# Kernel optimization log

Hardware: AMD Instinct MI355X
Metric: run time of the kernel (lower is better)

Reference implementation:

```python
import jax, jax.numpy as jnp
import numpy as np

T = 4096
STATE_DIM = 400
EMBED_DIM = 300
WIDTH_DIM = 20
HID = 150
GI_DIM = 2 * STATE_DIM + EMBED_DIM + WIDTH_DIM
BINS = (1, 2, 3, 4, 8, 16, 32, 64)
MAX_W = 10


def _dtoi(d):
    return sum(1 for b in BINS if d >= b)


def _mlp(x, W1, b1, W2, b2, W3, b3):
    h = jax.nn.relu(x @ W1 + b1)
    h = jax.nn.relu(h @ W2 + b2)
    return h @ W3 + b3


def setup_inputs() -> dict:
    key = jax.random.key(0)
    ks = jax.random.split(key, 16)
    s = 0.02
    return {
        "embeds": jax.random.normal(ks[0], (T, EMBED_DIM), jnp.float32),
        "states": jax.random.normal(ks[1], (T, STATE_DIM), jnp.float32),
        # attention Scorer (state_dim -> 150 -> 150 -> 1)
        "aW1": jax.random.normal(ks[2], (STATE_DIM, HID), jnp.float32) * s,
        "ab1": jnp.zeros((HID,), jnp.float32),
        "aW2": jax.random.normal(ks[3], (HID, HID), jnp.float32) * s,
        "ab2": jnp.zeros((HID,), jnp.float32),
        "aW3": jax.random.normal(ks[4], (HID, 1), jnp.float32) * s,
        "ab3": jnp.zeros((1,), jnp.float32),
        # width embedding table: len(BINS)+1 rows
        "width_table": jax.random.normal(ks[5], (len(BINS) + 1, WIDTH_DIM), jnp.float32) * s,
        # sm Scorer (gi_dim -> 150 -> 150 -> 1)
        "sW1": jax.random.normal(ks[6], (GI_DIM, HID), jnp.float32) * s,
        "sb1": jnp.zeros((HID,), jnp.float32),
        "sW2": jax.random.normal(ks[7], (HID, HID), jnp.float32) * s,
        "sb2": jnp.zeros((HID,), jnp.float32),
        "sW3": jax.random.normal(ks[8], (HID, 1), jnp.float32) * s,
        "sb3": jnp.zeros((1,), jnp.float32),
    }


def reference(embeds, states, aW1, ab1, aW2, ab2, aW3, ab3, width_table,
              sW1, sb1, sW2, sb2, sW3, sb3):
    t = states.shape[0]
    attn_scores = _mlp(states, aW1, ab1, aW2, ab2, aW3, ab3)[:, 0]  # [T]

    gs_parts, width_parts = [], []
    for n in range(1, MAX_W + 1):  # fixed, small window-size loop
        w = t - n + 1
        starts = jnp.arange(w)
        idx = starts[:, None] + jnp.arange(n)[None, :]        # [W, n]
        a = jax.nn.softmax(attn_scores[idx], axis=1)           # per-span softmax
        pooled = jnp.einsum('wn,wnd->wd', a, embeds[idx])      # [W, embed]
        g = jnp.concatenate([states[starts], states[starts + n - 1], pooled], axis=1)
        gs_parts.append(g)
        width_parts.append(width_table[_dtoi(n)][None, :].repeat(w, axis=0))

    gs = jnp.concatenate(gs_parts, axis=0)                     # [S, 2*state+embed]
    widths = jnp.concatenate(width_parts, axis=0)              # [S, width_dim]
    gs = jnp.concatenate([gs, widths], axis=1)                 # [S, gi_dim]
    sms = _mlp(gs, sW1, sb1, sW2, sb2, sW3, sb3)[:, 0]         # [S]
    return sms
```

## Files before the change

### kernel.cpp

```cpp
#include <hip/hip_runtime.h>
#include <hip/hip_bf16.h>

#define T_TOK 4096
#define HID   150
#define HPAD  160
#define NSPAN 40915
#define MAXW  10
#define NT    10

typedef __attribute__((ext_vector_type(8))) _Float16 f16x8;
typedef __attribute__((ext_vector_type(4))) float    f32x4;

__global__ __launch_bounds__(256) void k_prep(
    const float* __restrict__ aW1, const float* __restrict__ sW1,
    const float* __restrict__ aW2, const float* __restrict__ sW2,
    const float* __restrict__ wt, const float* __restrict__ sb1,
    _Float16* __restrict__ fW1, _Float16* __restrict__ fA1,
    _Float16* __restrict__ fB1, _Float16* __restrict__ fE1,
    _Float16* __restrict__ fA2, _Float16* __restrict__ fW2,
    float* __restrict__ wc)
{
    const int b = blockIdx.x;
    const int w = threadIdx.x >> 6, l = threadIdx.x & 63;

    if (b < 148) {
        int tw = b * 4 + w;
        if (tw >= 590) return;
        const float* src; int srcK, off; _Float16* d;
        if      (tw < 130) { src = aW1;             srcK = 400; off = 0;   d = fW1; }
        else if (tw < 260) { src = sW1;             srcK = 400; off = 130; d = fA1; }
        else if (tw < 390) { src = sW1 + 400 * HID; srcK = 400; off = 260; d = fB1; }
        else if (tw < 490) { src = sW1 + 800 * HID; srcK = 300; off = 390; d = fE1; }
        else if (tw < 540) { src = aW2;             srcK = 150; off = 490; d = fA2; }
        else               { src = sW2;             srcK = 150; off = 540; d = fW2; }
        int tb = tw - off;
        int kt = tb / NT, nt = tb - kt * NT;
        int n = nt * 16 + (l & 15);
        int kbase = kt * 32 + (l >> 4) * 8;
        f16x8 hv;
#pragma unroll
        for (int e = 0; e < 8; e++) {
            int k = kbase + e;
            float f = (k < srcK && n < HID) ? src[(size_t)k * HID + n] : 0.f;
            hv[e] = (_Float16)f;
        }
        *(f16x8*)(d + ((size_t)tb * 64 + l) * 8) = hv;
    } else {
        int n = b - 147;
        int c = threadIdx.x;
        if (c >= HPAD) return;
        float s = 0.f;
        if (c < HID) {
            const int dt[11] = {0, 1, 2, 3, 4, 4, 4, 4, 5, 5, 5};
            const float* ww = wt + dt[n] * 20;
            s = sb1[c];
#pragma unroll
            for (int j = 0; j < 20; j++) s = fmaf(ww[j], sW1[(1100 + j) * HID + c], s);
        }
        wc[(n - 1) * HPAD + c] = s;
    }
}

__global__ __launch_bounds__(256) void k_proj(
    const float* __restrict__ states, const float* __restrict__ embeds,
    const _Float16* __restrict__ fW1, const _Float16* __restrict__ fA1,
    const _Float16* __restrict__ fB1, const _Float16* __restrict__ fE1,
    const _Float16* __restrict__ fA2,
    const float* __restrict__ ab1, const float* __restrict__ ab2,
    const float* __restrict__ aW3, const float* __restrict__ ab3,
    _Float16* __restrict__ Abuf, _Float16* __restrict__ Bbuf,
    _Float16* __restrict__ Ebuf, float* __restrict__ scores)
{
    __shared__ alignas(16) _Float16 hh[5120];
    __shared__ float red[4][16];

    const float* Asrc; int lda, srcK, KT; const _Float16* Bf; _Float16* C = nullptr;
    switch (blockIdx.y) {
        case 0: Asrc = states; lda = 400; srcK = 400; KT = 13; Bf = fW1; break;
        case 1: Asrc = states; lda = 400; srcK = 400; KT = 13; Bf = fA1; C = Abuf; break;
        case 2: Asrc = states; lda = 400; srcK = 400; KT = 13; Bf = fB1; C = Bbuf; break;
        default:Asrc = embeds; lda = 300; srcK = 300; KT = 10; Bf = fE1; C = Ebuf; break;
    }
    const int w = threadIdx.x >> 6, l = threadIdx.x & 63;
    const int mtl = w >> 1;
    const int mt  = blockIdx.x * 2 + mtl;
    const int nh  = w & 1;
    const int m15 = l & 15;
    const int koff = (l >> 4) * 8;
    const float* arow = Asrc + (size_t)(mt * 16 + m15) * lda;
    const f16x8* pB = (const f16x8*)Bf;

    f32x4 acc[5];
#pragma unroll
    for (int c = 0; c < 5; c++) acc[c] = (f32x4){0.f, 0.f, 0.f, 0.f};

#pragma unroll 2
    for (int kt = 0; kt < KT; ++kt) {
        const int kbase = kt * 32 + koff;
        f16x8 a;
        if (kbase + 8 <= srcK) {
            float4 v0 = *(const float4*)(arow + kbase);
            float4 v1 = *(const float4*)(arow + kbase + 4);
            a[0] = (_Float16)v0.x; a[1] = (_Float16)v0.y;
            a[2] = (_Float16)v0.z; a[3] = (_Float16)v0.w;
            a[4] = (_Float16)v1.x; a[5] = (_Float16)v1.y;
            a[6] = (_Float16)v1.z; a[7] = (_Float16)v1.w;
        } else {
#pragma unroll
            for (int e = 0; e < 8; e++)
                a[e] = (_Float16)((kbase + e < srcK) ? arow[kbase + e] : 0.f);
        }
#pragma unroll
        for (int c = 0; c < 5; c++) {
            f16x8 bv = pB[(size_t)(kt * NT + nh * 5 + c) * 64 + l];
            acc[c] = __builtin_amdgcn_mfma_f32_16x16x32_f16(a, bv, acc[c], 0, 0, 0);
        }
    }

    if (blockIdx.y != 0) {
        const int m0 = mt * 16;
#pragma unroll
        for (int c = 0; c < 5; c++) {
            int col = (nh * 5 + c) * 16 + m15;
#pragma unroll
            for (int r = 0; r < 4; r++) {
                int row = m0 + (l >> 4) * 4 + r;
                C[(size_t)row * HPAD + col] = (_Float16)acc[c][r];
            }
        }
        return;
    }

#pragma unroll
    for (int c = 0; c < 5; c++) {
        int u   = nh * 5 + c;
        int col = u * 16 + m15;
        float bb = (col < HID) ? ab1[col] : 0.f;
        int kt = u >> 1;
        int g  = (u & 1) * 2 + (m15 >> 3);
        int e  = m15 & 7;
#pragma unroll
        for (int r = 0; r < 4; r++) {
            int rloc = (l >> 4) * 4 + r;
            float v = fmaxf(acc[c][r] + bb, 0.f);
            hh[((mtl * 5 + kt) * 64 + g * 16 + rloc) * 8 + e] = (_Float16)v;
        }
    }
    __syncthreads();

    const f16x8* pH = (const f16x8*)hh;
    const f16x8* pB2 = (const f16x8*)fA2;
    f32x4 acc2[5];
#pragma unroll
    for (int c = 0; c < 5; c++) acc2[c] = (f32x4){0.f, 0.f, 0.f, 0.f};
#pragma unroll
    for (int kt = 0; kt < 5; ++kt) {
        f16x8 a = pH[(mtl * 5 + kt) * 64 + l];
#pragma unroll
        for (int c = 0; c < 5; c++) {
            f16x8 bv = pB2[(size_t)(kt * NT + nh * 5 + c) * 64 + l];
            acc2[c] = __builtin_amdgcn_mfma_f32_16x16x32_f16(a, bv, acc2[c], 0, 0, 0);
        }
    }
    float p[4] = {0.f, 0.f, 0.f, 0.f};
#pragma unroll
    for (int c = 0; c < 5; c++) {
        int col = (nh * 5 + c) * 16 + m15;
        float bb = (col < HID) ? ab2[col] : 0.f;
        float wv = (col < HID) ? aW3[col] : 0.f;
#pragma unroll
        for (int r = 0; r < 4; r++) {
            float v = fmaxf(acc2[c][r] + bb, 0.f);
            p[r] = fmaf(v, wv, p[r]);
        }
    }
#pragma unroll
    for (int off = 1; off < 16; off <<= 1)
#pragma unroll
        for (int r = 0; r < 4; r++) p[r] += __shfl_xor(p[r], off);
    if (m15 == 0)
#pragma unroll
        for (int r = 0; r < 4; r++) red[w][(l >> 4) * 4 + r] = p[r];
    __syncthreads();
    if (threadIdx.x < 32) {
        int ml = threadIdx.x;
        scores[blockIdx.x * 32 + ml] =
            red[(ml >> 4) * 2 + 0][ml & 15] + red[(ml >> 4) * 2 + 1][ml & 15] + ab3[0];
    }
}

__global__ __launch_bounds__(256) void k_spanfinal(
    const float* __restrict__ scores, const _Float16* __restrict__ Abuf,
    const _Float16* __restrict__ Bbuf, const _Float16* __restrict__ Ebuf,
    const float* __restrict__ wc,
    const _Float16* __restrict__ fW2,
    const float* __restrict__ sb2, const float* __restrict__ sW3,
    const float* __restrict__ sb3, float* __restrict__ out)
{
    __shared__ alignas(16) _Float16 hh[5120];
    __shared__ float wg[32][10];
    __shared__ int   stI[32], nnI[32];
    __shared__ float red[4][16];

    const int tid = threadIdx.x;
    const int s0  = blockIdx.x * 32;

    if (tid < 32) {
        int span = s0 + tid;
        int n = 1, start = 0;
        if (span < NSPAN) {
            int base = 0;
#pragma unroll
            for (int i = 1; i <= MAXW; i++) {
                int ww = T_TOK - i + 1;
                if (span < base + ww) { n = i; break; }
                base += ww;
            }
            start = span - base;
        }
        float sc[MAXW]; float mx = -1e30f;
#pragma unroll
        for (int i = 0; i < MAXW; i++) {
            sc[i] = (i < n) ? scores[start + i] : -1e30f;
            mx = fmaxf(mx, sc[i]);
        }
        float ssum = 0.f;
#pragma unroll
        for (int i = 0; i < MAXW; i++) { sc[i] = __expf(sc[i] - mx); ssum += sc[i]; }
        float inv = 1.f / ssum;
#pragma unroll
        for (int i = 0; i < MAXW; i++) wg[tid][i] = (i < n) ? sc[i] * inv : 0.f;
        stI[tid] = start;
        nnI[tid] = n;
    }
    __syncthreads();

#pragma unroll
    for (int it = 0; it < 3; ++it) {
        int task = it * 256 + tid;
        if (task < 640) {
            int sl = task / 20;
            int q  = task - sl * 20;
            int start = stI[sl];
            int nn = nnI[sl];
            int d0 = q * 8;
            f16x8 a8 = *(const f16x8*)(Abuf + (size_t)start * HPAD + d0);
            f16x8 b8 = *(const f16x8*)(Bbuf + (size_t)(start + nn - 1) * HPAD + d0);
            const float* wr = wc + (nn - 1) * HPAD + d0;
            float v[8];
#pragma unroll
            for (int e = 0; e < 8; e++) v[e] = (float)a8[e] + (float)b8[e] + wr[e];
#pragma unroll
            for (int i = 0; i < MAXW; i++) {
                int ridx = min(start + i, T_TOK - 1);
                f16x8 e8 = *(const f16x8*)(Ebuf + (size_t)ridx * HPAD + d0);
                float aa = wg[sl][i];
#pragma unroll
                for (int e = 0; e < 8; e++) v[e] = fmaf(aa, (float)e8[e], v[e]);
            }
            f16x8 hv;
#pragma unroll
            for (int e = 0; e < 8; e++) hv[e] = (_Float16)fmaxf(v[e], 0.f);
            int mtl = sl >> 4, smr = sl & 15;
            int kt = q >> 2, gg = q & 3;
            *(f16x8*)(hh + ((mtl * 5 + kt) * 64 + gg * 16 + smr) * 8) = hv;
        }
    }
    __syncthreads();

    const int w = tid >> 6, l = tid & 63;
    const int mtl = w >> 1, nh = w & 1;
    const int m15 = l & 15;
    const f16x8* pH = (const f16x8*)hh;
    const f16x8* pB = (const f16x8*)fW2;
    f32x4 acc[5];
#pragma unroll
    for (int c = 0; c < 5; c++) acc[c] = (f32x4){0.f, 0.f, 0.f, 0.f};
#pragma unroll
    for (int kt = 0; kt < 5; ++kt) {
        f16x8 a = pH[(mtl * 5 + kt) * 64 + l];
#pragma unroll
        for (int c = 0; c < 5; c++) {
            f16x8 bv = pB[(size_t)(kt * NT + nh * 5 + c) * 64 + l];
            acc[c] = __builtin_amdgcn_mfma_f32_16x16x32_f16(a, bv, acc[c], 0, 0, 0);
        }
    }
    float p[4] = {0.f, 0.f, 0.f, 0.f};
#pragma unroll
    for (int c = 0; c < 5; c++) {
        int col = (nh * 5 + c) * 16 + m15;
        float bb = (col < HID) ? sb2[col] : 0.f;
        float wv = (col < HID) ? sW3[col] : 0.f;
#pragma unroll
        for (int r = 0; r < 4; r++) {
            float v = fmaxf(acc[c][r] + bb, 0.f);
            p[r] = fmaf(v, wv, p[r]);
        }
    }
#pragma unroll
    for (int off = 1; off < 16; off <<= 1)
#pragma unroll
        for (int r = 0; r < 4; r++) p[r] += __shfl_xor(p[r], off);
    if (m15 == 0)
#pragma unroll
        for (int r = 0; r < 4; r++) red[w][(l >> 4) * 4 + r] = p[r];
    __syncthreads();
    if (tid < 32) {
        int row = s0 + tid;
        if (row < NSPAN)
            out[row] = red[(tid >> 4) * 2 + 0][tid & 15] +
                       red[(tid >> 4) * 2 + 1][tid & 15] + sb3[0];
    }
}

extern "C" void kernel_launch(void* const* d_in, const int* in_sizes, int n_in,
                              void* d_out, int out_size, void* d_ws, size_t ws_size,
                              hipStream_t stream) {
    const float* embeds = (const float*)d_in[0];
    const float* states = (const float*)d_in[1];
    const float* aW1 = (const float*)d_in[2];
    const float* ab1 = (const float*)d_in[3];
    const float* aW2 = (const float*)d_in[4];
    const float* ab2 = (const float*)d_in[5];
    const float* aW3 = (const float*)d_in[6];
    const float* ab3 = (const float*)d_in[7];
    const float* wt  = (const float*)d_in[8];
    const float* sW1 = (const float*)d_in[9];
    const float* sb1 = (const float*)d_in[10];
    const float* sW2 = (const float*)d_in[11];
    const float* sb2 = (const float*)d_in[12];
    const float* sW3 = (const float*)d_in[13];
    const float* sb3 = (const float*)d_in[14];
    float* out = (float*)d_out;

    char* W = (char*)d_ws;
    _Float16* Abuf = (_Float16*)(W + 0);
    _Float16* Bbuf = (_Float16*)(W + 1310720);
    _Float16* Ebuf = (_Float16*)(W + 2621440);
    float* scores  = (float*)(W + 3932160);
    float* wcbuf   = (float*)(W + 3948544);
    _Float16* fW1  = (_Float16*)(W + 3954944);
    _Float16* fA1  = (_Float16*)(W + 4088064);
    _Float16* fB1  = (_Float16*)(W + 4221184);
    _Float16* fE1  = (_Float16*)(W + 4354304);
    _Float16* fA2  = (_Float16*)(W + 4456704);
    _Float16* fW2  = (_Float16*)(W + 4507904);

    k_prep<<<158, 256, 0, stream>>>(aW1, sW1, aW2, sW2, wt, sb1,
                                    fW1, fA1, fB1, fE1, fA2, fW2, wcbuf);
    k_proj<<<dim3(128, 4), 256, 0, stream>>>(states, embeds,
        fW1, fA1, fB1, fE1, fA2, ab1, ab2, aW3, ab3, Abuf, Bbuf, Ebuf, scores);
    k_spanfinal<<<1279, 256, 0, stream>>>(scores, Abuf, Bbuf, Ebuf, wcbuf,
        fW2, sb2, sW3, sb3, out);
}
```

Measured before the change: 38.42 us.

## Fuse projection and span-scoring kernels into one tile-local kernel with halo recompute

```diff
diff --git a/kernel.cpp b/kernel.cpp
--- a/kernel.cpp
+++ b/kernel.cpp
@@ -10,6 +10,23 @@
 
 typedef __attribute__((ext_vector_type(8))) _Float16 f16x8;
 typedef __attribute__((ext_vector_type(4))) float    f32x4;
+
+static __device__ __forceinline__ f16x8 cvt8(const float* __restrict__ row, int kbase, int K) {
+    f16x8 a;
+    if (kbase + 8 <= K) {
+        float4 v0 = *(const float4*)(row + kbase);
+        float4 v1 = *(const float4*)(row + kbase + 4);
+        a[0] = (_Float16)v0.x; a[1] = (_Float16)v0.y;
+        a[2] = (_Float16)v0.z; a[3] = (_Float16)v0.w;
+        a[4] = (_Float16)v1.x; a[5] = (_Float16)v1.y;
+        a[6] = (_Float16)v1.z; a[7] = (_Float16)v1.w;
+    } else {
+#pragma unroll
+        for (int e = 0; e < 8; e++)
+            a[e] = (_Float16)((kbase + e < K) ? row[kbase + e] : 0.f);
+    }
+    return a;
+}
 
 __global__ __launch_bounds__(256) void k_prep(
     const float* __restrict__ aW1, const float* __restrict__ sW1,
@@ -61,167 +78,160 @@
     }
 }
 
-__global__ __launch_bounds__(256) void k_proj(
+__global__ __launch_bounds__(256, 2) void k_main(
     const float* __restrict__ states, const float* __restrict__ embeds,
     const _Float16* __restrict__ fW1, const _Float16* __restrict__ fA1,
     const _Float16* __restrict__ fB1, const _Float16* __restrict__ fE1,
-    const _Float16* __restrict__ fA2,
+    const _Float16* __restrict__ fA2, const _Float16* __restrict__ fW2,
     const float* __restrict__ ab1, const float* __restrict__ ab2,
     const float* __restrict__ aW3, const float* __restrict__ ab3,
-    _Float16* __restrict__ Abuf, _Float16* __restrict__ Bbuf,
-    _Float16* __restrict__ Ebuf, float* __restrict__ scores)
+    const float* __restrict__ wcbuf, const float* __restrict__ sb2,
+    const float* __restrict__ sW3, const float* __restrict__ sb3,
+    float* __restrict__ out)
 {
-    __shared__ alignas(16) _Float16 hh[5120];
-    __shared__ float red[4][16];
-
-    const float* Asrc; int lda, srcK, KT; const _Float16* Bf; _Float16* C = nullptr;
-    switch (blockIdx.y) {
-        case 0: Asrc = states; lda = 400; srcK = 400; KT = 13; Bf = fW1; break;
-        case 1: Asrc = states; lda = 400; srcK = 400; KT = 13; Bf = fA1; C = Abuf; break;
-        case 2: Asrc = states; lda = 400; srcK = 400; KT = 13; Bf = fB1; C = Bbuf; break;
-        default:Asrc = embeds; lda = 300; srcK = 300; KT = 10; Bf = fE1; C = Ebuf; break;
-    }
-    const int w = threadIdx.x >> 6, l = threadIdx.x & 63;
-    const int mtl = w >> 1;
-    const int mt  = blockIdx.x * 2 + mtl;
-    const int nh  = w & 1;
-    const int m15 = l & 15;
+    __shared__ alignas(16) char smem[71808];
+    _Float16* Sf    = (_Float16*)(smem);
+    _Float16* Atile = (_Float16*)(smem + 26624);
+    _Float16* Btile = (_Float16*)(smem + 36864);
+    _Float16* Etile = (_Float16*)(smem + 47104);
+    _Float16* hh1   = (_Float16*)(smem + 57344);
+    float*    wg    = (float*)   (smem + 67584);
+    float*    scl   = (float*)   (smem + 70784);
+    float*    red   = (float*)   (smem + 70912);
+    float*    redB  = (float*)   (smem + 71552);
+
+    const int tid  = threadIdx.x;
+    const int w    = tid >> 6, l = tid & 63;
+    const int mtl  = w >> 1, nh = w & 1, m15 = l & 15;
     const int koff = (l >> 4) * 8;
-    const float* arow = Asrc + (size_t)(mt * 16 + m15) * lda;
-    const f16x8* pB = (const f16x8*)Bf;
-
-    f32x4 acc[5];
-#pragma unroll
-    for (int c = 0; c < 5; c++) acc[c] = (f32x4){0.f, 0.f, 0.f, 0.f};
-
+    const int t0   = blockIdx.x * 8;
+
+    for (int ft = w; ft < 26; ft += 4) {
+        int mt2 = ft / 13, kt = ft - mt2 * 13;
+        int row = min(t0 + mt2 * 16 + m15, T_TOK - 1);
+        f16x8 a = cvt8(states + (size_t)row * 400, kt * 32 + koff, 400);
+        *(f16x8*)(Sf + ((size_t)ft * 64 + l) * 8) = a;
+    }
+    __syncthreads();
+
+    for (int g = 0; g < 3; ++g) {
+        const f16x8* pB = (const f16x8*)(g == 0 ? fW1 : (g == 1 ? fA1 : fB1));
+        f32x4 acc[5];
+#pragma unroll
+        for (int c = 0; c < 5; c++) acc[c] = (f32x4){0.f, 0.f, 0.f, 0.f};
+#pragma unroll
+        for (int kt = 0; kt < 13; ++kt) {
+            f16x8 a = *(const f16x8*)(Sf + (((mtl * 13 + kt) * 64) + l) * 8);
+#pragma unroll
+            for (int c = 0; c < 5; c++) {
+                f16x8 bv = pB[(size_t)(kt * NT + nh * 5 + c) * 64 + l];
+                acc[c] = __builtin_amdgcn_mfma_f32_16x16x32_f16(a, bv, acc[c], 0, 0, 0);
+            }
+        }
+        if (g == 0) {
+#pragma unroll
+            for (int c = 0; c < 5; c++) {
+                int u = nh * 5 + c;
+                int col = u * 16 + m15;
+                float bb = (col < HID) ? ab1[col] : 0.f;
+                int kt2 = u >> 1;
+                int gg = (u & 1) * 2 + (m15 >> 3);
+                int e = m15 & 7;
+#pragma unroll
+                for (int r = 0; r < 4; r++) {
+                    int rloc = (l >> 4) * 4 + r;
+                    float v = fmaxf(acc[c][r] + bb, 0.f);
+                    hh1[((mtl * 5 + kt2) * 64 + gg * 16 + rloc) * 8 + e] = (_Float16)v;
+                }
+            }
+        } else {
+            _Float16* Tt = (g == 1) ? Atile : Btile;
+#pragma unroll
+            for (int c = 0; c < 5; c++) {
+                int col = (nh * 5 + c) * 16 + m15;
+#pragma unroll
+                for (int r = 0; r < 4; r++) {
+                    int rr = mtl * 16 + (l >> 4) * 4 + r;
+                    Tt[rr * HPAD + col] = (_Float16)acc[c][r];
+                }
+            }
+        }
+    }
+    {
+        f32x4 acc[5];
+#pragma unroll
+        for (int c = 0; c < 5; c++) acc[c] = (f32x4){0.f, 0.f, 0.f, 0.f};
+        int row = min(t0 + mtl * 16 + m15, T_TOK - 1);
+        const float* arow = embeds + (size_t)row * 300;
 #pragma unroll 2
-    for (int kt = 0; kt < KT; ++kt) {
-        const int kbase = kt * 32 + koff;
-        f16x8 a;
-        if (kbase + 8 <= srcK) {
-            float4 v0 = *(const float4*)(arow + kbase);
-            float4 v1 = *(const float4*)(arow + kbase + 4);
-            a[0] = (_Float16)v0.x; a[1] = (_Float16)v0.y;
-            a[2] = (_Float16)v0.z; a[3] = (_Float16)v0.w;
-            a[4] = (_Float16)v1.x; a[5] = (_Float16)v1.y;
-            a[6] = (_Float16)v1.z; a[7] = (_Float16)v1.w;
-        } else {
-#pragma unroll
-            for (int e = 0; e < 8; e++)
-                a[e] = (_Float16)((kbase + e < srcK) ? arow[kbase + e] : 0.f);
-        }
-#pragma unroll
-        for (int c = 0; c < 5; c++) {
-            f16x8 bv = pB[(size_t)(kt * NT + nh * 5 + c) * 64 + l];
-            acc[c] = __builtin_amdgcn_mfma_f32_16x16x32_f16(a, bv, acc[c], 0, 0, 0);
-        }
-    }
-
-    if (blockIdx.y != 0) {
-        const int m0 = mt * 16;
+        for (int kt = 0; kt < 10; ++kt) {
+            f16x8 a = cvt8(arow, kt * 32 + koff, 300);
+#pragma unroll
+            for (int c = 0; c < 5; c++) {
+                f16x8 bv = ((const f16x8*)fE1)[(size_t)(kt * NT + nh * 5 + c) * 64 + l];
+                acc[c] = __builtin_amdgcn_mfma_f32_16x16x32_f16(a, bv, acc[c], 0, 0, 0);
+            }
+        }
 #pragma unroll
         for (int c = 0; c < 5; c++) {
             int col = (nh * 5 + c) * 16 + m15;
 #pragma unroll
             for (int r = 0; r < 4; r++) {
-                int row = m0 + (l >> 4) * 4 + r;
-                C[(size_t)row * HPAD + col] = (_Float16)acc[c][r];
-            }
-        }
-        return;
-    }
-
-#pragma unroll
-    for (int c = 0; c < 5; c++) {
-        int u   = nh * 5 + c;
-        int col = u * 16 + m15;
-        float bb = (col < HID) ? ab1[col] : 0.f;
-        int kt = u >> 1;
-        int g  = (u & 1) * 2 + (m15 >> 3);
-        int e  = m15 & 7;
-#pragma unroll
-        for (int r = 0; r < 4; r++) {
-            int rloc = (l >> 4) * 4 + r;
-            float v = fmaxf(acc[c][r] + bb, 0.f);
-            hh[((mtl * 5 + kt) * 64 + g * 16 + rloc) * 8 + e] = (_Float16)v;
-        }
-    }
-    __syncthreads();
-
-    const f16x8* pH = (const f16x8*)hh;
-    const f16x8* pB2 = (const f16x8*)fA2;
-    f32x4 acc2[5];
-#pragma unroll
-    for (int c = 0; c < 5; c++) acc2[c] = (f32x4){0.f, 0.f, 0.f, 0.f};
-#pragma unroll
-    for (int kt = 0; kt < 5; ++kt) {
-        f16x8 a = pH[(mtl * 5 + kt) * 64 + l];
+                int rr = mtl * 16 + (l >> 4) * 4 + r;
+                Etile[rr * HPAD + col] = (_Float16)acc[c][r];
+            }
+        }
+    }
+    __syncthreads();
+
+    {
+        f32x4 acc2[5];
+#pragma unroll
+        for (int c = 0; c < 5; c++) acc2[c] = (f32x4){0.f, 0.f, 0.f, 0.f};
+        const f16x8* pH = (const f16x8*)hh1;
+        const f16x8* pB2 = (const f16x8*)fA2;
+#pragma unroll
+        for (int kt = 0; kt < 5; ++kt) {
+            f16x8 a = pH[(mtl * 5 + kt) * 64 + l];
+#pragma unroll
+            for (int c = 0; c < 5; c++) {
+                f16x8 bv = pB2[(size_t)(kt * NT + nh * 5 + c) * 64 + l];
+                acc2[c] = __builtin_amdgcn_mfma_f32_16x16x32_f16(a, bv, acc2[c], 0, 0, 0);
+            }
+        }
+        float p[4] = {0.f, 0.f, 0.f, 0.f};
 #pragma unroll
         for (int c = 0; c < 5; c++) {
-            f16x8 bv = pB2[(size_t)(kt * NT + nh * 5 + c) * 64 + l];
-            acc2[c] = __builtin_amdgcn_mfma_f32_16x16x32_f16(a, bv, acc2[c], 0, 0, 0);
-        }
-    }
-    float p[4] = {0.f, 0.f, 0.f, 0.f};
-#pragma unroll
-    for (int c = 0; c < 5; c++) {
-        int col = (nh * 5 + c) * 16 + m15;
-        float bb = (col < HID) ? ab2[col] : 0.f;
-        float wv = (col < HID) ? aW3[col] : 0.f;
-#pragma unroll
-        for (int r = 0; r < 4; r++) {
-            float v = fmaxf(acc2[c][r] + bb, 0.f);
-            p[r] = fmaf(v, wv, p[r]);
-        }
-    }
-#pragma unroll
-    for (int off = 1; off < 16; off <<= 1)
-#pragma unroll
-        for (int r = 0; r < 4; r++) p[r] += __shfl_xor(p[r], off);
-    if (m15 == 0)
-#pragma unroll
-        for (int r = 0; r < 4; r++) red[w][(l >> 4) * 4 + r] = p[r];
-    __syncthreads();
-    if (threadIdx.x < 32) {
-        int ml = threadIdx.x;
-        scores[blockIdx.x * 32 + ml] =
-            red[(ml >> 4) * 2 + 0][ml & 15] + red[(ml >> 4) * 2 + 1][ml & 15] + ab3[0];
-    }
-}
-
-__global__ __launch_bounds__(256) void k_spanfinal(
-    const float* __restrict__ scores, const _Float16* __restrict__ Abuf,
-    const _Float16* __restrict__ Bbuf, const _Float16* __restrict__ Ebuf,
-    const float* __restrict__ wc,
-    const _Float16* __restrict__ fW2,
-    const float* __restrict__ sb2, const float* __restrict__ sW3,
-    const float* __restrict__ sb3, float* __restrict__ out)
-{
-    __shared__ alignas(16) _Float16 hh[5120];
-    __shared__ float wg[32][10];
-    __shared__ int   stI[32], nnI[32];
-    __shared__ float red[4][16];
-
-    const int tid = threadIdx.x;
-    const int s0  = blockIdx.x * 32;
-
-    if (tid < 32) {
-        int span = s0 + tid;
-        int n = 1, start = 0;
-        if (span < NSPAN) {
-            int base = 0;
-#pragma unroll
-            for (int i = 1; i <= MAXW; i++) {
-                int ww = T_TOK - i + 1;
-                if (span < base + ww) { n = i; break; }
-                base += ww;
-            }
-            start = span - base;
-        }
+            int col = (nh * 5 + c) * 16 + m15;
+            float bb = (col < HID) ? ab2[col] : 0.f;
+            float wv = (col < HID) ? aW3[col] : 0.f;
+#pragma unroll
+            for (int r = 0; r < 4; r++) {
+                float v = fmaxf(acc2[c][r] + bb, 0.f);
+                p[r] = fmaf(v, wv, p[r]);
+            }
+        }
+#pragma unroll
+        for (int off = 1; off < 16; off <<= 1)
+#pragma unroll
+            for (int r = 0; r < 4; r++) p[r] += __shfl_xor(p[r], off);
+        if (m15 == 0)
+#pragma unroll
+            for (int r = 0; r < 4; r++) redB[w * 16 + (l >> 4) * 4 + r] = p[r];
+        __syncthreads();
+        if (tid < 32)
+            scl[tid] = redB[((tid >> 4) * 2 + 0) * 16 + (tid & 15)] +
+                       redB[((tid >> 4) * 2 + 1) * 16 + (tid & 15)] + ab3[0];
+    }
+    __syncthreads();
+
+    if (tid < 80) {
+        int ni = tid >> 3, si = tid & 7;
+        int n = ni + 1;
         float sc[MAXW]; float mx = -1e30f;
 #pragma unroll
         for (int i = 0; i < MAXW; i++) {
-            sc[i] = (i < n) ? scores[start + i] : -1e30f;
+            sc[i] = (i < n) ? scl[si + i] : -1e30f;
             mx = fmaxf(mx, sc[i]);
         }
         float ssum = 0.f;
@@ -229,87 +239,95 @@
         for (int i = 0; i < MAXW; i++) { sc[i] = __expf(sc[i] - mx); ssum += sc[i]; }
         float inv = 1.f / ssum;
 #pragma unroll
-        for (int i = 0; i < MAXW; i++) wg[tid][i] = (i < n) ? sc[i] * inv : 0.f;
-        stI[tid] = start;
-        nnI[tid] = n;
-    }
-    __syncthreads();
-
-#pragma unroll
-    for (int it = 0; it < 3; ++it) {
+        for (int i = 0; i < MAXW; i++) wg[tid * 10 + i] = (i < n) ? sc[i] * inv : 0.f;
+    }
+    __syncthreads();
+
+#pragma unroll
+    for (int it = 0; it < 7; ++it) {
         int task = it * 256 + tid;
-        if (task < 640) {
-            int sl = task / 20;
-            int q  = task - sl * 20;
-            int start = stI[sl];
-            int nn = nnI[sl];
+        if (task < 1600) {
+            int sl = task / 20, q = task - sl * 20;
+            int ni = sl >> 3, si = sl & 7;
             int d0 = q * 8;
-            f16x8 a8 = *(const f16x8*)(Abuf + (size_t)start * HPAD + d0);
-            f16x8 b8 = *(const f16x8*)(Bbuf + (size_t)(start + nn - 1) * HPAD + d0);
-            const float* wr = wc + (nn - 1) * HPAD + d0;
+            f16x8 a8 = *(const f16x8*)(Atile + si * HPAD + d0);
+            f16x8 b8 = *(const f16x8*)(Btile + (si + ni) * HPAD + d0);
+            float4 w4a = *(const float4*)(wcbuf + ni * HPAD + d0);
+            float4 w4b = *(const float4*)(wcbuf + ni * HPAD + d0 + 4);
             float v[8];
-#pragma unroll
-            for (int e = 0; e < 8; e++) v[e] = (float)a8[e] + (float)b8[e] + wr[e];
+            v[0] = (float)a8[0] + (float)b8[0] + w4a.x;
+            v[1] = (float)a8[1] + (float)b8[1] + w4a.y;
+            v[2] = (float)a8[2] + (float)b8[2] + w4a.z;
+            v[3] = (float)a8[3] + (float)b8[3] + w4a.w;
+            v[4] = (float)a8[4] + (float)b8[4] + w4b.x;
+            v[5] = (float)a8[5] + (float)b8[5] + w4b.y;
+            v[6] = (float)a8[6] + (float)b8[6] + w4b.z;
+            v[7] = (float)a8[7] + (float)b8[7] + w4b.w;
 #pragma unroll
             for (int i = 0; i < MAXW; i++) {
-                int ridx = min(start + i, T_TOK - 1);
-                f16x8 e8 = *(const f16x8*)(Ebuf + (size_t)ridx * HPAD + d0);
-                float aa = wg[sl][i];
+                f16x8 e8 = *(const f16x8*)(Etile + (si + i) * HPAD + d0);
+                float aa = wg[sl * 10 + i];
 #pragma unroll
                 for (int e = 0; e < 8; e++) v[e] = fmaf(aa, (float)e8[e], v[e]);
             }
             f16x8 hv;
 #pragma unroll
             for (int e = 0; e < 8; e++) hv[e] = (_Float16)fmaxf(v[e], 0.f);
-            int mtl = sl >> 4, smr = sl & 15;
+            int mti = sl >> 4, rr = sl & 15;
             int kt = q >> 2, gg = q & 3;
-            *(f16x8*)(hh + ((mtl * 5 + kt) * 64 + gg * 16 + smr) * 8) = hv;
-        }
-    }
-    __syncthreads();
-
-    const int w = tid >> 6, l = tid & 63;
-    const int mtl = w >> 1, nh = w & 1;
-    const int m15 = l & 15;
-    const f16x8* pH = (const f16x8*)hh;
-    const f16x8* pB = (const f16x8*)fW2;
-    f32x4 acc[5];
-#pragma unroll
-    for (int c = 0; c < 5; c++) acc[c] = (f32x4){0.f, 0.f, 0.f, 0.f};
-#pragma unroll
-    for (int kt = 0; kt < 5; ++kt) {
-        f16x8 a = pH[(mtl * 5 + kt) * 64 + l];
-#pragma unroll
-        for (int c = 0; c < 5; c++) {
-            f16x8 bv = pB[(size_t)(kt * NT + nh * 5 + c) * 64 + l];
-            acc[c] = __builtin_amdgcn_mfma_f32_16x16x32_f16(a, bv, acc[c], 0, 0, 0);
-        }
-    }
-    float p[4] = {0.f, 0.f, 0.f, 0.f};
-#pragma unroll
-    for (int c = 0; c < 5; c++) {
-        int col = (nh * 5 + c) * 16 + m15;
-        float bb = (col < HID) ? sb2[col] : 0.f;
-        float wv = (col < HID) ? sW3[col] : 0.f;
-#pragma unroll
-        for (int r = 0; r < 4; r++) {
-            float v = fmaxf(acc[c][r] + bb, 0.f);
-            p[r] = fmaf(v, wv, p[r]);
-        }
-    }
-#pragma unroll
-    for (int off = 1; off < 16; off <<= 1)
-#pragma unroll
-        for (int r = 0; r < 4; r++) p[r] += __shfl_xor(p[r], off);
-    if (m15 == 0)
-#pragma unroll
-        for (int r = 0; r < 4; r++) red[w][(l >> 4) * 4 + r] = p[r];
-    __syncthreads();
-    if (tid < 32) {
-        int row = s0 + tid;
-        if (row < NSPAN)
-            out[row] = red[(tid >> 4) * 2 + 0][tid & 15] +
-                       red[(tid >> 4) * 2 + 1][tid & 15] + sb3[0];
+            *(f16x8*)(Sf + (((mti * 5 + kt) * 64 + gg * 16 + rr) * 8)) = hv;
+        }
+    }
+    __syncthreads();
+
+    {
+        const f16x8* pW2 = (const f16x8*)fW2;
+        for (int mti = (w >> 1); mti < 5; mti += 2) {
+            f32x4 acc[5];
+#pragma unroll
+            for (int c = 0; c < 5; c++) acc[c] = (f32x4){0.f, 0.f, 0.f, 0.f};
+#pragma unroll
+            for (int kt = 0; kt < 5; ++kt) {
+                f16x8 a = *(const f16x8*)(Sf + (((mti * 5 + kt) * 64) + l) * 8);
+#pragma unroll
+                for (int c = 0; c < 5; c++) {
+                    f16x8 bv = pW2[(size_t)(kt * NT + nh * 5 + c) * 64 + l];
+                    acc[c] = __builtin_amdgcn_mfma_f32_16x16x32_f16(a, bv, acc[c], 0, 0, 0);
+                }
+            }
+            float p[4] = {0.f, 0.f, 0.f, 0.f};
+#pragma unroll
+            for (int c = 0; c < 5; c++) {
+                int col = (nh * 5 + c) * 16 + m15;
+                float bb = (col < HID) ? sb2[col] : 0.f;
+                float wv = (col < HID) ? sW3[col] : 0.f;
+#pragma unroll
+                for (int r = 0; r < 4; r++) {
+                    float v = fmaxf(acc[c][r] + bb, 0.f);
+                    p[r] = fmaf(v, wv, p[r]);
+                }
+            }
+#pragma unroll
+            for (int off = 1; off < 16; off <<= 1)
+#pragma unroll
+                for (int r = 0; r < 4; r++) p[r] += __shfl_xor(p[r], off);
+            if (m15 == 0)
+#pragma unroll
+                for (int r = 0; r < 4; r++)
+                    red[(nh * 5 + mti) * 16 + (l >> 4) * 4 + r] = p[r];
+        }
+    }
+    __syncthreads();
+
+    if (tid < 80) {
+        int mti = tid >> 4, rr = tid & 15;
+        float val = red[(0 * 5 + mti) * 16 + rr] + red[(1 * 5 + mti) * 16 + rr] + sb3[0];
+        int ni = tid >> 3, si = tid & 7;
+        int start = t0 + si, n = ni + 1;
+        if (start + n <= T_TOK) {
+            int base = ni * (T_TOK + 1) - (ni * (ni + 1)) / 2;
+            out[base + start] = val;
+        }
     }
 }
 
@@ -334,22 +352,17 @@
     float* out = (float*)d_out;
 
     char* W = (char*)d_ws;
-    _Float16* Abuf = (_Float16*)(W + 0);
-    _Float16* Bbuf = (_Float16*)(W + 1310720);
-    _Float16* Ebuf = (_Float16*)(W + 2621440);
-    float* scores  = (float*)(W + 3932160);
-    float* wcbuf   = (float*)(W + 3948544);
-    _Float16* fW1  = (_Float16*)(W + 3954944);
-    _Float16* fA1  = (_Float16*)(W + 4088064);
-    _Float16* fB1  = (_Float16*)(W + 4221184);
-    _Float16* fE1  = (_Float16*)(W + 4354304);
-    _Float16* fA2  = (_Float16*)(W + 4456704);
-    _Float16* fW2  = (_Float16*)(W + 4507904);
+    _Float16* fW1  = (_Float16*)(W + 0);
+    _Float16* fA1  = (_Float16*)(W + 133120);
+    _Float16* fB1  = (_Float16*)(W + 266240);
+    _Float16* fE1  = (_Float16*)(W + 399360);
+    _Float16* fA2  = (_Float16*)(W + 501760);
+    _Float16* fW2  = (_Float16*)(W + 552960);
+    float*    wcbuf= (float*)   (W + 604160);
 
     k_prep<<<158, 256, 0, stream>>>(aW1, sW1, aW2, sW2, wt, sb1,
                                     fW1, fA1, fB1, fE1, fA2, fW2, wcbuf);
-    k_proj<<<dim3(128, 4), 256, 0, stream>>>(states, embeds,
-        fW1, fA1, fB1, fE1, fA2, ab1, ab2, aW3, ab3, Abuf, Bbuf, Ebuf, scores);
-    k_spanfinal<<<1279, 256, 0, stream>>>(scores, Abuf, Bbuf, Ebuf, wcbuf,
-        fW2, sb2, sW3, sb3, out);
+    k_main<<<512, 256, 0, stream>>>(states, embeds,
+        fW1, fA1, fB1, fE1, fA2, fW2,
+        ab1, ab2, aW3, ab3, wcbuf, sb2, sW3, sb3, out);
 }
```

Result: slower. 54.81 us (+42.6%).

## Split K across wave pairs in projection kernel and parallelize span softmax

Applied to the files above, without the earlier changes.

```diff
diff --git a/kernel.cpp b/kernel.cpp
--- a/kernel.cpp
+++ b/kernel.cpp
@@ -10,6 +10,23 @@
 
 typedef __attribute__((ext_vector_type(8))) _Float16 f16x8;
 typedef __attribute__((ext_vector_type(4))) float    f32x4;
+
+static __device__ __forceinline__ f16x8 cvt8(const float* __restrict__ row, int kbase, int K) {
+    f16x8 a;
+    if (kbase + 8 <= K) {
+        float4 v0 = *(const float4*)(row + kbase);
+        float4 v1 = *(const float4*)(row + kbase + 4);
+        a[0] = (_Float16)v0.x; a[1] = (_Float16)v0.y;
+        a[2] = (_Float16)v0.z; a[3] = (_Float16)v0.w;
+        a[4] = (_Float16)v1.x; a[5] = (_Float16)v1.y;
+        a[6] = (_Float16)v1.z; a[7] = (_Float16)v1.w;
+    } else {
+#pragma unroll
+        for (int e = 0; e < 8; e++)
+            a[e] = (_Float16)((kbase + e < K) ? row[kbase + e] : 0.f);
+    }
+    return a;
+}
 
 __global__ __launch_bounds__(256) void k_prep(
     const float* __restrict__ aW1, const float* __restrict__ sW1,
@@ -61,7 +78,7 @@
     }
 }
 
-__global__ __launch_bounds__(256) void k_proj(
+__global__ __launch_bounds__(512) void k_proj(
     const float* __restrict__ states, const float* __restrict__ embeds,
     const _Float16* __restrict__ fW1, const _Float16* __restrict__ fA1,
     const _Float16* __restrict__ fB1, const _Float16* __restrict__ fE1,
@@ -71,6 +88,7 @@
     _Float16* __restrict__ Abuf, _Float16* __restrict__ Bbuf,
     _Float16* __restrict__ Ebuf, float* __restrict__ scores)
 {
+    __shared__ float smP[256 * 21];
     __shared__ alignas(16) _Float16 hh[5120];
     __shared__ float red[4][16];
 
@@ -81,111 +99,156 @@
         case 2: Asrc = states; lda = 400; srcK = 400; KT = 13; Bf = fB1; C = Bbuf; break;
         default:Asrc = embeds; lda = 300; srcK = 300; KT = 10; Bf = fE1; C = Ebuf; break;
     }
-    const int w = threadIdx.x >> 6, l = threadIdx.x & 63;
-    const int mtl = w >> 1;
+    const int tid = threadIdx.x;
+    const int w   = tid >> 6, l = tid & 63;
+    const int mtl = w >> 2;
+    const int nh  = (w >> 1) & 1;
+    const int kh  = w & 1;
     const int mt  = blockIdx.x * 2 + mtl;
-    const int nh  = w & 1;
     const int m15 = l & 15;
     const int koff = (l >> 4) * 8;
     const float* arow = Asrc + (size_t)(mt * 16 + m15) * lda;
     const f16x8* pB = (const f16x8*)Bf;
+    const int pid = (mtl * 2 + nh) * 64 + l;
 
     f32x4 acc[5];
 #pragma unroll
     for (int c = 0; c < 5; c++) acc[c] = (f32x4){0.f, 0.f, 0.f, 0.f};
 
-#pragma unroll 2
-    for (int kt = 0; kt < KT; ++kt) {
-        const int kbase = kt * 32 + koff;
-        f16x8 a;
-        if (kbase + 8 <= srcK) {
-            float4 v0 = *(const float4*)(arow + kbase);
-            float4 v1 = *(const float4*)(arow + kbase + 4);
-            a[0] = (_Float16)v0.x; a[1] = (_Float16)v0.y;
-            a[2] = (_Float16)v0.z; a[3] = (_Float16)v0.w;
-            a[4] = (_Float16)v1.x; a[5] = (_Float16)v1.y;
-            a[6] = (_Float16)v1.z; a[7] = (_Float16)v1.w;
+    if (KT == 13) {
+        if (kh == 0) {
+#pragma unroll
+            for (int kt = 0; kt < 7; ++kt) {
+                f16x8 a = cvt8(arow, kt * 32 + koff, 400);
+#pragma unroll
+                for (int c = 0; c < 5; c++) {
+                    f16x8 bv = pB[(size_t)(kt * NT + nh * 5 + c) * 64 + l];
+                    acc[c] = __builtin_amdgcn_mfma_f32_16x16x32_f16(a, bv, acc[c], 0, 0, 0);
+                }
+            }
         } else {
 #pragma unroll
-            for (int e = 0; e < 8; e++)
-                a[e] = (_Float16)((kbase + e < srcK) ? arow[kbase + e] : 0.f);
-        }
+            for (int kt = 7; kt < 13; ++kt) {
+                f16x8 a = cvt8(arow, kt * 32 + koff, 400);
+#pragma unroll
+                for (int c = 0; c < 5; c++) {
+                    f16x8 bv = pB[(size_t)(kt * NT + nh * 5 + c) * 64 + l];
+                    acc[c] = __builtin_amdgcn_mfma_f32_16x16x32_f16(a, bv, acc[c], 0, 0, 0);
+                }
+            }
+        }
+    } else {
+        if (kh == 0) {
+#pragma unroll
+            for (int kt = 0; kt < 5; ++kt) {
+                f16x8 a = cvt8(arow, kt * 32 + koff, 300);
+#pragma unroll
+                for (int c = 0; c < 5; c++) {
+                    f16x8 bv = pB[(size_t)(kt * NT + nh * 5 + c) * 64 + l];
+                    acc[c] = __builtin_amdgcn_mfma_f32_16x16x32_f16(a, bv, acc[c], 0, 0, 0);
+                }
+            }
+        } else {
+#pragma unroll
+            for (int kt = 5; kt < 10; ++kt) {
+                f16x8 a = cvt8(arow, kt * 32 + koff, 300);
+#pragma unroll
+                for (int c = 0; c < 5; c++) {
+                    f16x8 bv = pB[(size_t)(kt * NT + nh * 5 + c) * 64 + l];
+                    acc[c] = __builtin_amdgcn_mfma_f32_16x16x32_f16(a, bv, acc[c], 0, 0, 0);
+                }
+            }
+        }
+    }
+
+    if (kh == 1) {
+#pragma unroll
+        for (int c = 0; c < 5; c++)
+#pragma unroll
+            for (int r = 0; r < 4; r++) smP[pid * 21 + c * 4 + r] = acc[c][r];
+    }
+    __syncthreads();
+    if (kh == 0) {
+#pragma unroll
+        for (int c = 0; c < 5; c++)
+#pragma unroll
+            for (int r = 0; r < 4; r++) acc[c][r] += smP[pid * 21 + c * 4 + r];
+    }
+
+    if (blockIdx.y != 0) {
+        if (kh == 0) {
+            const int m0 = mt * 16;
+#pragma unroll
+            for (int c = 0; c < 5; c++) {
+                int col = (nh * 5 + c) * 16 + m15;
+#pragma unroll
+                for (int r = 0; r < 4; r++) {
+                    int row = m0 + (l >> 4) * 4 + r;
+                    C[(size_t)row * HPAD + col] = (_Float16)acc[c][r];
+                }
+            }
+        }
+        return;
+    }
+
+    if (kh == 0) {
 #pragma unroll
         for (int c = 0; c < 5; c++) {
-            f16x8 bv = pB[(size_t)(kt * NT + nh * 5 + c) * 64 + l];
-            acc[c] = __builtin_amdgcn_mfma_f32_16x16x32_f16(a, bv, acc[c], 0, 0, 0);
-        }
-    }
-
-    if (blockIdx.y != 0) {
-        const int m0 = mt * 16;
+            int u   = nh * 5 + c;
+            int col = u * 16 + m15;
+            float bb = (col < HID) ? ab1[col] : 0.f;
+            int kt2 = u >> 1;
+            int g  = (u & 1) * 2 + (m15 >> 3);
+            int e  = m15 & 7;
+#pragma unroll
+            for (int r = 0; r < 4; r++) {
+                int rloc = (l >> 4) * 4 + r;
+                float v = fmaxf(acc[c][r] + bb, 0.f);
+                hh[((mtl * 5 + kt2) * 64 + g * 16 + rloc) * 8 + e] = (_Float16)v;
+            }
+        }
+    }
+    __syncthreads();
+
+    if (kh == 0) {
+        const f16x8* pH = (const f16x8*)hh;
+        const f16x8* pB2 = (const f16x8*)fA2;
+        f32x4 acc2[5];
+#pragma unroll
+        for (int c = 0; c < 5; c++) acc2[c] = (f32x4){0.f, 0.f, 0.f, 0.f};
+#pragma unroll
+        for (int kt = 0; kt < 5; ++kt) {
+            f16x8 a = pH[(mtl * 5 + kt) * 64 + l];
+#pragma unroll
+            for (int c = 0; c < 5; c++) {
+                f16x8 bv = pB2[(size_t)(kt * NT + nh * 5 + c) * 64 + l];
+                acc2[c] = __builtin_amdgcn_mfma_f32_16x16x32_f16(a, bv, acc2[c], 0, 0, 0);
+            }
+        }
+        float p[4] = {0.f, 0.f, 0.f, 0.f};
 #pragma unroll
         for (int c = 0; c < 5; c++) {
             int col = (nh * 5 + c) * 16 + m15;
+            float bb = (col < HID) ? ab2[col] : 0.f;
+            float wv = (col < HID) ? aW3[col] : 0.f;
 #pragma unroll
             for (int r = 0; r < 4; r++) {
-                int row = m0 + (l >> 4) * 4 + r;
-                C[(size_t)row * HPAD + col] = (_Float16)acc[c][r];
-            }
-        }
-        return;
-    }
-
-#pragma unroll
-    for (int c = 0; c < 5; c++) {
-        int u   = nh * 5 + c;
-        int col = u * 16 + m15;
-        float bb = (col < HID) ? ab1[col] : 0.f;
-        int kt = u >> 1;
-        int g  = (u & 1) * 2 + (m15 >> 3);
-        int e  = m15 & 7;
-#pragma unroll
-        for (int r = 0; r < 4; r++) {
-            int rloc = (l >> 4) * 4 + r;
-            float v = fmaxf(acc[c][r] + bb, 0.f);
-            hh[((mtl * 5 + kt) * 64 + g * 16 + rloc) * 8 + e] = (_Float16)v;
-        }
-    }
-    __syncthreads();
-
-    const f16x8* pH = (const f16x8*)hh;
-    const f16x8* pB2 = (const f16x8*)fA2;
-    f32x4 acc2[5];
-#pragma unroll
-    for (int c = 0; c < 5; c++) acc2[c] = (f32x4){0.f, 0.f, 0.f, 0.f};
-#pragma unroll
-    for (int kt = 0; kt < 5; ++kt) {
-        f16x8 a = pH[(mtl * 5 + kt) * 64 + l];
-#pragma unroll
-        for (int c = 0; c < 5; c++) {
-            f16x8 bv = pB2[(size_t)(kt * NT + nh * 5 + c) * 64 + l];
-            acc2[c] = __builtin_amdgcn_mfma_f32_16x16x32_f16(a, bv, acc2[c], 0, 0, 0);
-        }
-    }
-    float p[4] = {0.f, 0.f, 0.f, 0.f};
-#pragma unroll
-    for (int c = 0; c < 5; c++) {
-        int col = (nh * 5 + c) * 16 + m15;
-        float bb = (col < HID) ? ab2[col] : 0.f;
-        float wv = (col < HID) ? aW3[col] : 0.f;
-#pragma unroll
-        for (int r = 0; r < 4; r++) {
-            float v = fmaxf(acc2[c][r] + bb, 0.f);
-            p[r] = fmaf(v, wv, p[r]);
-        }
-    }
-#pragma unroll
-    for (int off = 1; off < 16; off <<= 1)
-#pragma unroll
-        for (int r = 0; r < 4; r++) p[r] += __shfl_xor(p[r], off);
-    if (m15 == 0)
-#pragma unroll
-        for (int r = 0; r < 4; r++) red[w][(l >> 4) * 4 + r] = p[r];
-    __syncthreads();
-    if (threadIdx.x < 32) {
-        int ml = threadIdx.x;
-        scores[blockIdx.x * 32 + ml] =
-            red[(ml >> 4) * 2 + 0][ml & 15] + red[(ml >> 4) * 2 + 1][ml & 15] + ab3[0];
+                float v = fmaxf(acc2[c][r] + bb, 0.f);
+                p[r] = fmaf(v, wv, p[r]);
+            }
+        }
+#pragma unroll
+        for (int off = 1; off < 16; off <<= 1)
+#pragma unroll
+            for (int r = 0; r < 4; r++) p[r] += __shfl_xor(p[r], off);
+        if (m15 == 0)
+#pragma unroll
+            for (int r = 0; r < 4; r++) red[mtl * 2 + nh][(l >> 4) * 4 + r] = p[r];
+    }
+    __syncthreads();
+    if (tid < 32) {
+        scores[blockIdx.x * 32 + tid] =
+            red[(tid >> 4) * 2 + 0][tid & 15] + red[(tid >> 4) * 2 + 1][tid & 15] + ab3[0];
     }
 }
 
@@ -205,8 +268,9 @@
     const int tid = threadIdx.x;
     const int s0  = blockIdx.x * 32;
 
-    if (tid < 32) {
-        int span = s0 + tid;
+    {
+        int sl = tid >> 3, k = tid & 7;
+        int span = s0 + sl;
         int n = 1, start = 0;
         if (span < NSPAN) {
             int base = 0;
@@ -218,20 +282,21 @@
             }
             start = span - base;
         }
-        float sc[MAXW]; float mx = -1e30f;
-#pragma unroll
-        for (int i = 0; i < MAXW; i++) {
-            sc[i] = (i < n) ? scores[start + i] : -1e30f;
-            mx = fmaxf(mx, sc[i]);
-        }
-        float ssum = 0.f;
-#pragma unroll
-        for (int i = 0; i < MAXW; i++) { sc[i] = __expf(sc[i] - mx); ssum += sc[i]; }
-        float inv = 1.f / ssum;
-#pragma unroll
-        for (int i = 0; i < MAXW; i++) wg[tid][i] = (i < n) ? sc[i] * inv : 0.f;
-        stI[tid] = start;
-        nnI[tid] = n;
+        float x0 = (k < n)     ? scores[start + k]     : -1e30f;
+        float x1 = (k + 8 < n) ? scores[start + k + 8] : -1e30f;
+        float m = fmaxf(x0, x1);
+        m = fmaxf(m, __shfl_xor(m, 1));
+        m = fmaxf(m, __shfl_xor(m, 2));
+        m = fmaxf(m, __shfl_xor(m, 4));
+        float e0 = __expf(x0 - m), e1 = __expf(x1 - m);
+        float s = e0 + e1;
+        s += __shfl_xor(s, 1);
+        s += __shfl_xor(s, 2);
+        s += __shfl_xor(s, 4);
+        float inv = 1.f / s;
+        wg[sl][k] = e0 * inv;
+        if (k < 2) wg[sl][k + 8] = e1 * inv;
+        if (k == 0) { stI[sl] = start; nnI[sl] = n; }
     }
     __syncthreads();
 
@@ -348,7 +413,7 @@
 
     k_prep<<<158, 256, 0, stream>>>(aW1, sW1, aW2, sW2, wt, sb1,
                                     fW1, fA1, fB1, fE1, fA2, fW2, wcbuf);
-    k_proj<<<dim3(128, 4), 256, 0, stream>>>(states, embeds,
+    k_proj<<<dim3(128, 4), 512, 0, stream>>>(states, embeds,
         fW1, fA1, fB1, fE1, fA2, ab1, ab2, aW3, ab3, Abuf, Bbuf, Ebuf, scores);
     k_spanfinal<<<1279, 256, 0, stream>>>(scores, Abuf, Bbuf, Ebuf, wcbuf,
         fW2, sb2, sW3, sb3, out);
```

Result: faster. 37.60 us, median of 2 (-2.1%).
